# Optimization experiments

Measured on AMD Instinct MI355X. Metric: run time of the kernel, lower is better.

## Reference

```python
import jax, jax.numpy as jnp
import numpy as np

B, N, E = 2, 50000, 400000
FIN, HID, OUT = 128, 128, 128
EPS = 1e-5  # BatchNorm1d default eps


def setup_inputs() -> dict:
    key = jax.random.key(0)
    ks = jax.random.split(key, 12)
    x = jax.random.normal(ks[0], (B, N, FIN), dtype=jnp.float32)
    row = jax.random.randint(ks[1], (E,), 0, N, dtype=jnp.int32)          # scatter dst
    col = jnp.concatenate([jnp.arange(N, dtype=jnp.int32),                # ensure deg>=1
                           jax.random.randint(ks[2], (E - N,), 0, N, dtype=jnp.int32)])
    edge_index = jnp.stack([row, col])                                    # [2, E]
    deg = jnp.zeros((N,), jnp.float32).at[col].add(1.0)                   # degree(col, N)
    dis = deg ** -0.5
    norm = (dis[row] * dis[col])[None, :, None]                           # [1, E, 1]
    W1 = jax.random.normal(ks[3], (HID, FIN), jnp.float32) / np.sqrt(FIN)
    b1 = jax.random.normal(ks[4], (HID,), jnp.float32) * 0.01
    g1 = jnp.ones((N,), jnp.float32)
    be1 = jnp.zeros((N,), jnp.float32)
    W2 = jax.random.normal(ks[5], (OUT, HID), jnp.float32) / np.sqrt(HID)
    b2 = jax.random.normal(ks[6], (OUT,), jnp.float32) * 0.01
    g2 = jnp.ones((N,), jnp.float32)
    be2 = jnp.zeros((N,), jnp.float32)
    return {"x": x, "edge_index": edge_index, "norm": norm,
            "W1": W1, "b1": b1, "g1": g1, "be1": be1,
            "W2": W2, "b2": b2, "g2": g2, "be2": be2}


def _gcn_layer(x, edge_index, norm, W, b, g, be):
    # Linear (dropout p=0 -> identity)
    h = jnp.einsum('bnf,of->bno', x, W) + b                 # [B, N, C]
    # BatchNorm1d(num_features=N): per-node stats over (batch, channel)
    mu = jnp.mean(h, axis=(0, 2), keepdims=True)            # [1, N, 1]
    var = jnp.var(h, axis=(0, 2), keepdims=True)            # biased, as torch
    y = g[None, :, None] * (h - mu) * jax.lax.rsqrt(var + EPS) + be[None, :, None]
    a = jax.nn.gelu(y, approximate=False)                   # torch GELU = exact erf
    # message passing: gather src nodes, scale by norm, scatter-add to dst
    msgs = a[:, edge_index[1], :] * norm                    # [B, E, C]
    return jnp.zeros_like(a).at[:, edge_index[0], :].add(msgs)


def reference(x, edge_index, norm, W1, b1, g1, be1, W2, b2, g2, be2):
    x = _gcn_layer(x, edge_index, norm, W1, b1, g1, be1)
    x = _gcn_layer(x, edge_index, norm, W2, b2, g2, be2)
    return x
```

## Files before the change

kernel.cpp:

```cpp
#include <hip/hip_runtime.h>
#include <math.h>

#define CC 128

typedef unsigned short u16;
typedef short bf16x8 __attribute__((ext_vector_type(8)));
typedef float f32x4 __attribute__((ext_vector_type(4)));

typedef __attribute__((address_space(3))) void lds_t;
typedef const __attribute__((address_space(1))) void gbl_t;

__device__ __forceinline__ u16 f2bf(float f) {
    union { float f; unsigned u; } v; v.f = f;
    unsigned u = v.u;
    return (u16)((u + 0x7FFFu + ((u >> 16) & 1u)) >> 16);
}
__device__ __forceinline__ float bf2f(unsigned hi16) {
    union { unsigned u; float f; } v; v.u = hi16 << 16; return v.f;
}
__device__ __forceinline__ unsigned cvt_pk(float lo, float hi) {
    unsigned r;
    asm("v_cvt_pk_bf16_f32 %0, %1, %2" : "=v"(r) : "v"(lo), "v"(hi));
    return r;
}

__device__ __forceinline__ float gelu_f(float y) {
    float xa = fabsf(y) * 0.70710678118654752f;
    float t  = __builtin_amdgcn_rcpf(fmaf(0.3275911f, xa, 1.0f));
    float p  = fmaf(1.061405429f, t, -1.453152027f);
    p = fmaf(p, t, 1.421413741f);
    p = fmaf(p, t, -0.284496736f);
    p = fmaf(p, t, 0.254829592f);
    p *= t;
    float e  = __expf(-xa * xa);
    float er = fmaf(-p, e, 1.0f);
    float s  = copysignf(er, y);
    return 0.5f * y * (1.0f + s);
}


__global__ __launch_bounds__(256) void k_zero_i32(int* __restrict__ p, int n) {
    int i = blockIdx.x * 256 + threadIdx.x;
    if (i < n) p[i] = 0;
}

__global__ __launch_bounds__(256) void k_hist(const int* __restrict__ row, int* __restrict__ cnt, int E) {
    int e = blockIdx.x * 256 + threadIdx.x;
    if (e < E) atomicAdd(&cnt[row[e]], 1);
}

__device__ __forceinline__ int wave_incl_scan(int v) {
    #pragma unroll
    for (int d = 1; d < 64; d <<= 1) {
        int t = __shfl_up(v, d);
        if ((threadIdx.x & 63) >= d) v += t;
    }
    return v;
}

__global__ __launch_bounds__(256) void k_scan_a(const int* __restrict__ cnt, int* __restrict__ bsum, int N) {
    int base = blockIdx.x * 1024 + threadIdx.x * 4;
    int s = 0;
    #pragma unroll
    for (int u = 0; u < 4; ++u) { int i = base + u; if (i < N) s += cnt[i]; }
    #pragma unroll
    for (int d = 32; d > 0; d >>= 1) s += __shfl_down(s, d);
    __shared__ int wsum[4];
    if ((threadIdx.x & 63) == 0) wsum[threadIdx.x >> 6] = s;
    __syncthreads();
    if (threadIdx.x == 0) bsum[blockIdx.x] = wsum[0] + wsum[1] + wsum[2] + wsum[3];
}

__global__ __launch_bounds__(64) void k_scan_b(const int* __restrict__ bsum, int* __restrict__ boff,
                                               int* __restrict__ off, int N, int nb) {
    int carry = 0;
    for (int base = 0; base < nb; base += 64) {
        int t = base + (int)threadIdx.x;
        int v = (t < nb) ? bsum[t] : 0;
        int incl = wave_incl_scan(v);
        if (t < nb) boff[t] = carry + incl - v;
        carry += __shfl(incl, 63);
    }
    if (threadIdx.x == 0) off[N] = carry;
}

__global__ __launch_bounds__(256) void k_scan_c(int* __restrict__ cnt, const int* __restrict__ boff,
                                                int* __restrict__ off, int N) {
    int t = threadIdx.x;
    int base = blockIdx.x * 1024 + t * 4;
    int v[4]; int s = 0;
    #pragma unroll
    for (int u = 0; u < 4; ++u) { int i = base + u; v[u] = (i < N) ? cnt[i] : 0; s += v[u]; }
    int incl = wave_incl_scan(s);
    __shared__ int wsum[4];
    int w = t >> 6, lane = t & 63;
    if (lane == 63) wsum[w] = incl;
    __syncthreads();
    int run = incl - s + boff[blockIdx.x];
    for (int ww = 0; ww < w; ++ww) run += wsum[ww];
    #pragma unroll
    for (int u = 0; u < 4; ++u) {
        int i = base + u;
        if (i < N) { off[i] = run; cnt[i] = 0; }
        run += v[u];
    }
}

__global__ __launch_bounds__(256) void k_fill(const int* __restrict__ row, const int* __restrict__ col,
                                              const float* __restrict__ nrm, const int* __restrict__ off,
                                              int* __restrict__ cur, int2* __restrict__ eg, int E) {
    int e = blockIdx.x * 256 + threadIdx.x;
    if (e < E) {
        int r = row[e];
        int p = off[r] + atomicAdd(&cur[r], 1);
        eg[p] = make_int2(col[e], __float_as_int(nrm[e]));
    }
}

__global__ __launch_bounds__(256) void k_wrepack(const float* __restrict__ W1, u16* __restrict__ Wp1,
                                                 const float* __restrict__ W2, u16* __restrict__ Wp2) {
    int i = blockIdx.x * 256 + threadIdx.x;
    if (i < 2 * CC * CC) {
        int is2 = (i >= CC * CC);
        int ii = is2 ? i - CC * CC : i;
        int j = ii & 7, l = (ii >> 3) & 63, s = (ii >> 9) & 3, t = ii >> 11;
        int r = 16 * t + (l & 15);
        int p = s * 32 + ((l >> 4) & 3) * 8 + j;
        if (is2) {
            int k = (p & 7) * 16 + (p >> 3);
            Wp2[ii] = f2bf(W2[r * CC + k]);
        } else {
            Wp1[ii] = f2bf(W1[r * CC + p]);
        }
    }
}

__global__ __launch_bounds__(256) void k_fused_l1(
    const float* __restrict__ X, const u16* __restrict__ Wp1, const u16* __restrict__ Wp2,
    const float* __restrict__ bias, const float* __restrict__ gamma, const float* __restrict__ beta,
    u16* __restrict__ Z, int N)
{
    __shared__ __align__(16) u16 WS[CC * CC];
    __shared__ __align__(16) unsigned TT[4][16][68];

    const int tid = threadIdx.x;
    const int w = tid >> 6;
    const int l = tid & 63;
    const int g = l >> 4;
    const int c = l & 15;
    const int n8 = blockIdx.x * 32 + w * 8;
    const bool valid = n8 < N;
    const int nbase = valid ? n8 : 0;

    #pragma unroll
    for (int it = 0; it < 8; ++it) {
        const u16* gsrc = Wp1 + it * 2048 + w * 512 + l * 8;
        u16* ldst = &WS[it * 2048 + w * 512];
        __builtin_amdgcn_global_load_lds((gbl_t*)gsrc, (lds_t*)ldst, 16, 0, 0);
    }

    const int ab = c >> 3;
    const int an = nbase + (c & 7);
    const float* xbase = X + ((size_t)ab * N + an) * CC + g * 8;
    bf16x8 af[4];
    #pragma unroll
    for (int s = 0; s < 4; ++s) {
        float4 lo = *(const float4*)(xbase + s * 32);
        float4 hi = *(const float4*)(xbase + s * 32 + 4);
        unsigned aw[4];
        aw[0] = cvt_pk(lo.x, lo.y); aw[1] = cvt_pk(lo.z, lo.w);
        aw[2] = cvt_pk(hi.x, hi.y); aw[3] = cvt_pk(hi.z, hi.w);
        af[s] = *(bf16x8*)aw;
    }

    float bb[8];
    #pragma unroll
    for (int t = 0; t < 8; ++t) bb[t] = bias[t * 16 + c];
    float gam[4], bet[4];
    #pragma unroll
    for (int r = 0; r < 4; ++r) {
        int p = (4 * g + r) & 7;
        gam[r] = gamma[nbase + p];
        bet[r] = beta[nbase + p];
    }

    __syncthreads();

    f32x4 acc[8];
    #pragma unroll
    for (int t = 0; t < 8; ++t) acc[t] = (f32x4){0.f, 0.f, 0.f, 0.f};
    #pragma unroll
    for (int s = 0; s < 4; ++s) {
        bf16x8 bf[8];
        #pragma unroll
        for (int t = 0; t < 8; ++t)
            bf[t] = *(const bf16x8*)&WS[((t * 4 + s) * 64 + l) * 8];
        #pragma unroll
        for (int t = 0; t < 8; ++t)
            acc[t] = __builtin_amdgcn_mfma_f32_16x16x32_bf16(af[s], bf[t], acc[t], 0, 0, 0);
    }

    __syncthreads();

    #pragma unroll
    for (int it = 0; it < 8; ++it) {
        const u16* gsrc = Wp2 + it * 2048 + w * 512 + l * 8;
        u16* ldst = &WS[it * 2048 + w * 512];
        __builtin_amdgcn_global_load_lds((gbl_t*)gsrc, (lds_t*)ldst, 16, 0, 0);
    }

    float rs[4] = {0.f, 0.f, 0.f, 0.f}, rq[4] = {0.f, 0.f, 0.f, 0.f};
    #pragma unroll
    for (int t = 0; t < 8; ++t)
        #pragma unroll
        for (int r = 0; r < 4; ++r) {
            float h = acc[t][r] + bb[t];
            acc[t][r] = h;
            rs[r] += h;
            rq[r] += h * h;
        }
    #pragma unroll
    for (int d = 1; d < 16; d <<= 1) {
        #pragma unroll
        for (int r = 0; r < 4; ++r) {
            rs[r] += __shfl_xor(rs[r], d);
            rq[r] += __shfl_xor(rq[r], d);
        }
    }
    #pragma unroll
    for (int r = 0; r < 4; ++r) {
        rs[r] += __shfl_xor(rs[r], 32);
        rq[r] += __shfl_xor(rq[r], 32);
    }

    #pragma unroll
    for (int r = 0; r < 4; ++r) {
        float mean = rs[r] * (1.f / 256.f);
        float var  = rq[r] * (1.f / 256.f) - mean * mean;
        float sc = gam[r] * rsqrtf(fmaxf(var, 0.f) + 1e-5f);
        float sh = bet[r] - mean * sc;
        #pragma unroll
        for (int t = 0; t < 8; ++t)
            acc[t][r] = gelu_f(acc[t][r] * sc + sh);
    }

    #pragma unroll
    for (int r = 0; r < 4; ++r) {
        unsigned tw[4];
        #pragma unroll
        for (int tt = 0; tt < 4; ++tt)
            tw[tt] = cvt_pk(acc[2 * tt][r], acc[2 * tt + 1][r]);
        *(uint4*)&TT[w][4 * g + r][c * 4] = *(uint4*)tw;
    }
    bf16x8 af2[4];
    #pragma unroll
    for (int s = 0; s < 4; ++s)
        af2[s] = *(const bf16x8*)&TT[w][c][s * 16 + g * 4];

    __syncthreads();

    f32x4 acc2[8];
    #pragma unroll
    for (int t = 0; t < 8; ++t) acc2[t] = (f32x4){0.f, 0.f, 0.f, 0.f};
    #pragma unroll
    for (int s = 0; s < 4; ++s) {
        bf16x8 bf[8];
        #pragma unroll
        for (int t = 0; t < 8; ++t)
            bf[t] = *(const bf16x8*)&WS[((t * 4 + s) * 64 + l) * 8];
        #pragma unroll
        for (int t = 0; t < 8; ++t)
            acc2[t] = __builtin_amdgcn_mfma_f32_16x16x32_bf16(af2[s], bf[t], acc2[t], 0, 0, 0);
    }

    if (valid) {
        #pragma unroll
        for (int r = 0; r < 4; ++r) {
            int rr = 4 * g + r;
            int db = rr >> 3, dn = n8 + (rr & 7);
            unsigned zw[4];
            #pragma unroll
            for (int tt = 0; tt < 4; ++tt)
                zw[tt] = cvt_pk(acc2[2 * tt][r], acc2[2 * tt + 1][r]);
            *(uint4*)(Z + ((size_t)dn * 2 + db) * CC + c * 8) = *(uint4*)zw;
        }
    }
}

__global__ __launch_bounds__(256) void k_agg_bn(
    const u16* __restrict__ Zin, const int* __restrict__ off, const int2* __restrict__ eg,
    const float* __restrict__ b2, const float* __restrict__ g2, const float* __restrict__ be2,
    u16* __restrict__ A2, int N)
{
    __shared__ u16 TW[4][2][256];
    const int wv = threadIdx.x >> 6;
    const int l = threadIdx.x & 63;
    const int half = l >> 5;
    const int h = l & 31;
    const int b = h >> 4;
    const int c = h & 15;
    const int n = blockIdx.x * 8 + wv * 2 + half;
    const bool nv = n < N;
    const int nn = nv ? n : 0;
    const u16* Ab = Zin + b * CC + c * 8;

    float bb[8];
    #pragma unroll
    for (int t = 0; t < 8; ++t) bb[t] = b2[t * 16 + c];

    int s = off[nn];
    int e = nv ? off[nn + 1] : 0;
    float a[8] = {0.f, 0.f, 0.f, 0.f, 0.f, 0.f, 0.f, 0.f};
    for (int j = s; j < e; j += 4) {
        int2 e0 = eg[j], e1 = eg[j + 1], e2 = eg[j + 2], e3 = eg[j + 3];
        int s0 = e0.x;                  float w0 = __int_as_float(e0.y);
        int s1 = (j + 1 < e) ? e1.x : 0; float w1 = (j + 1 < e) ? __int_as_float(e1.y) : 0.f;
        int s2 = (j + 2 < e) ? e2.x : 0; float w2 = (j + 2 < e) ? __int_as_float(e2.y) : 0.f;
        int s3 = (j + 3 < e) ? e3.x : 0; float w3 = (j + 3 < e) ? __int_as_float(e3.y) : 0.f;
        bf16x8 v0 = *(const bf16x8*)(Ab + (size_t)s0 * 256);
        bf16x8 v1 = *(const bf16x8*)(Ab + (size_t)s1 * 256);
        bf16x8 v2 = *(const bf16x8*)(Ab + (size_t)s2 * 256);
        bf16x8 v3 = *(const bf16x8*)(Ab + (size_t)s3 * 256);
        #pragma unroll
        for (int q = 0; q < 8; ++q) {
            a[q] = fmaf(w0, bf2f((u16)v0[q]), a[q]);
            a[q] = fmaf(w1, bf2f((u16)v1[q]), a[q]);
            a[q] = fmaf(w2, bf2f((u16)v2[q]), a[q]);
            a[q] = fmaf(w3, bf2f((u16)v3[q]), a[q]);
        }
    }

    float ss = 0.f, qq = 0.f;
    #pragma unroll
    for (int t = 0; t < 8; ++t) {
        float hh = a[t] + bb[t];
        a[t] = hh;
        ss += hh;
        qq += hh * hh;
    }
    #pragma unroll
    for (int d = 1; d < 32; d <<= 1) {
        ss += __shfl_xor(ss, d);
        qq += __shfl_xor(qq, d);
    }
    float mean = ss * (1.f / 256.f);
    float var  = qq * (1.f / 256.f) - mean * mean;
    float sc = g2[nn] * rsqrtf(fmaxf(var, 0.f) + 1e-5f);
    float sh = be2[nn] - mean * sc;

    #pragma unroll
    for (int t = 0; t < 8; ++t)
        TW[wv][half][b * CC + t * 16 + c] = f2bf(gelu_f(a[t] * sc + sh));
    if (nv) {
        bf16x8 v = *(const bf16x8*)&TW[wv][half][h * 8];
        *(bf16x8*)(A2 + (size_t)nn * 256 + h * 8) = v;
    }
}

__global__ __launch_bounds__(256) void k_agg_out(
    const u16* __restrict__ A2, const int* __restrict__ off, const int2* __restrict__ eg,
    float* __restrict__ Out, int N)
{
    const int wv = threadIdx.x >> 6;
    const int l = threadIdx.x & 63;
    const int half = l >> 5;
    const int h = l & 31;
    const int b = h >> 4;
    const int c = h & 15;
    const int n = blockIdx.x * 8 + wv * 2 + half;
    const bool nv = n < N;
    const int nn = nv ? n : 0;
    const u16* Ab = A2 + h * 8;

    int s = off[nn];
    int e = nv ? off[nn + 1] : 0;
    float a[8] = {0.f, 0.f, 0.f, 0.f, 0.f, 0.f, 0.f, 0.f};
    for (int j = s; j < e; j += 4) {
        int2 e0 = eg[j], e1 = eg[j + 1], e2 = eg[j + 2], e3 = eg[j + 3];
        int s0 = e0.x;                  float w0 = __int_as_float(e0.y);
        int s1 = (j + 1 < e) ? e1.x : 0; float w1 = (j + 1 < e) ? __int_as_float(e1.y) : 0.f;
        int s2 = (j + 2 < e) ? e2.x : 0; float w2 = (j + 2 < e) ? __int_as_float(e2.y) : 0.f;
        int s3 = (j + 3 < e) ? e3.x : 0; float w3 = (j + 3 < e) ? __int_as_float(e3.y) : 0.f;
        bf16x8 v0 = *(const bf16x8*)(Ab + (size_t)s0 * 256);
        bf16x8 v1 = *(const bf16x8*)(Ab + (size_t)s1 * 256);
        bf16x8 v2 = *(const bf16x8*)(Ab + (size_t)s2 * 256);
        bf16x8 v3 = *(const bf16x8*)(Ab + (size_t)s3 * 256);
        #pragma unroll
        for (int q = 0; q < 8; ++q) {
            a[q] = fmaf(w0, bf2f((u16)v0[q]), a[q]);
            a[q] = fmaf(w1, bf2f((u16)v1[q]), a[q]);
            a[q] = fmaf(w2, bf2f((u16)v2[q]), a[q]);
            a[q] = fmaf(w3, bf2f((u16)v3[q]), a[q]);
        }
    }
    if (nv) {
        float* d = Out + ((size_t)b * N + nn) * CC + c * 8;
        *(float4*)&d[0] = make_float4(a[0], a[1], a[2], a[3]);
        *(float4*)&d[4] = make_float4(a[4], a[5], a[6], a[7]);
    }
}


extern "C" void kernel_launch(void* const* d_in, const int* in_sizes, int n_in,
                              void* d_out, int out_size, void* d_ws, size_t ws_size,
                              hipStream_t stream)
{
    const float* x   = (const float*)d_in[0];
    const int*   ei  = (const int*)d_in[1];
    const float* nrm = (const float*)d_in[2];
    const float* W1  = (const float*)d_in[3];
    const float* b1  = (const float*)d_in[4];
    const float* g1  = (const float*)d_in[5];
    const float* be1 = (const float*)d_in[6];
    const float* W2  = (const float*)d_in[7];
    const float* b2  = (const float*)d_in[8];
    const float* g2  = (const float*)d_in[9];
    const float* be2 = (const float*)d_in[10];

    const int N = in_sizes[5];
    const int E = in_sizes[2];
    const int* row = ei;
    const int* col = ei + E;
    const int nb = (N + 1023) / 1024;

    auto al = [](size_t v) { return (v + 255) & ~(size_t)255; };
    char* p = (char*)d_ws;
    int* off    = (int*)p;   p += al((size_t)(N + 1) * 4);
    int* cur    = (int*)p;   p += al((size_t)N * 4);
    int2* eg    = (int2*)p;  p += al((size_t)(E + 8) * 8);
    int* bsum   = (int*)p;   p += al((size_t)nb * 4);
    int* boff   = (int*)p;   p += al((size_t)nb * 4);
    u16* Wp1    = (u16*)p;   p += al((size_t)CC * CC * 2);
    u16* Wp2    = (u16*)p;   p += al((size_t)CC * CC * 2);
    u16* Zbuf   = (u16*)p;   p += al((size_t)2 * N * CC * 2);
    u16* A2buf  = (u16*)p;   p += al((size_t)2 * N * CC * 2);

    k_zero_i32<<<(N + 255) / 256, 256, 0, stream>>>(cur, N);
    k_hist<<<(E + 255) / 256, 256, 0, stream>>>(row, cur, E);
    k_scan_a<<<nb, 256, 0, stream>>>(cur, bsum, N);
    k_scan_b<<<1, 64, 0, stream>>>(bsum, boff, off, N, nb);
    k_scan_c<<<nb, 256, 0, stream>>>(cur, boff, off, N);
    k_fill<<<(E + 255) / 256, 256, 0, stream>>>(row, col, nrm, off, cur, eg, E);

    k_wrepack<<<(2 * CC * CC + 255) / 256, 256, 0, stream>>>(W1, Wp1, W2, Wp2);

    const int gb = (N + 31) / 32;
    const int ga = (N + 7) / 8;
    k_fused_l1<<<gb, 256, 0, stream>>>(x, Wp1, Wp2, b1, g1, be1, Zbuf, N);
    k_agg_bn<<<ga, 256, 0, stream>>>(Zbuf, off, eg, b2, g2, be2, A2buf, N);
    k_agg_out<<<ga, 256, 0, stream>>>(A2buf, off, eg, (float*)d_out, N);
}
```

Baseline: 153.2 us.

## Make fused layer-1 kernel persistent with resident weights and X prefetch

The fused linear/BN/GELU/linear kernel becomes persistent: 512 blocks loop over node tiles, keeping both repacked weight matrices in separate LDS buffers so they load once per block instead of once per tile. The next tile's X, gamma and beta are prefetched into registers while the current tile computes, and the transpose scratch uses an XOR swizzle instead of padding to avoid bank conflicts. The zeroing and weight-repack kernels are merged into one launch. The trade-offs are higher LDS and register use per block (launch_bounds 256,2) and a fixed grid size that may not match the CU count.

```diff
diff --git a/kernel.cpp b/kernel.cpp
--- a/kernel.cpp
+++ b/kernel.cpp
@@ -39,11 +39,6 @@
 }
 
 
-__global__ __launch_bounds__(256) void k_zero_i32(int* __restrict__ p, int n) {
-    int i = blockIdx.x * 256 + threadIdx.x;
-    if (i < n) p[i] = 0;
-}
-
 __global__ __launch_bounds__(256) void k_hist(const int* __restrict__ row, int* __restrict__ cnt, int E) {
     int e = blockIdx.x * 256 + threadIdx.x;
     if (e < E) atomicAdd(&cnt[row[e]], 1);
@@ -117,12 +112,15 @@
     }
 }
 
-__global__ __launch_bounds__(256) void k_wrepack(const float* __restrict__ W1, u16* __restrict__ Wp1,
-                                                 const float* __restrict__ W2, u16* __restrict__ Wp2) {
+__global__ __launch_bounds__(256) void k_prep(int* __restrict__ cur, int N,
+                                              const float* __restrict__ W1, u16* __restrict__ Wp1,
+                                              const float* __restrict__ W2, u16* __restrict__ Wp2) {
     int i = blockIdx.x * 256 + threadIdx.x;
-    if (i < 2 * CC * CC) {
-        int is2 = (i >= CC * CC);
-        int ii = is2 ? i - CC * CC : i;
+    if (i < N) { cur[i] = 0; return; }
+    int iw = i - N;
+    if (iw < 2 * CC * CC) {
+        int is2 = (iw >= CC * CC);
+        int ii = is2 ? iw - CC * CC : iw;
         int j = ii & 7, l = (ii >> 3) & 63, s = (ii >> 9) & 3, t = ii >> 11;
         int r = 16 * t + (l & 15);
         int p = s * 32 + ((l >> 4) & 3) * 8 + j;
@@ -135,154 +133,166 @@
     }
 }
 
-__global__ __launch_bounds__(256) void k_fused_l1(
+__global__ __launch_bounds__(256, 2) void k_fused_l1(
     const float* __restrict__ X, const u16* __restrict__ Wp1, const u16* __restrict__ Wp2,
     const float* __restrict__ bias, const float* __restrict__ gamma, const float* __restrict__ beta,
     u16* __restrict__ Z, int N)
 {
-    __shared__ __align__(16) u16 WS[CC * CC];
-    __shared__ __align__(16) unsigned TT[4][16][68];
+    __shared__ __align__(16) u16 WS1[CC * CC];
+    __shared__ __align__(16) u16 WS2[CC * CC];
+    __shared__ __align__(16) unsigned TT[4][16][64];
 
     const int tid = threadIdx.x;
     const int w = tid >> 6;
     const int l = tid & 63;
     const int g = l >> 4;
     const int c = l & 15;
-    const int n8 = blockIdx.x * 32 + w * 8;
-    const bool valid = n8 < N;
-    const int nbase = valid ? n8 : 0;
+    const int ntiles = (N + 31) / 32;
+    const int NB = gridDim.x;
 
     #pragma unroll
     for (int it = 0; it < 8; ++it) {
-        const u16* gsrc = Wp1 + it * 2048 + w * 512 + l * 8;
-        u16* ldst = &WS[it * 2048 + w * 512];
-        __builtin_amdgcn_global_load_lds((gbl_t*)gsrc, (lds_t*)ldst, 16, 0, 0);
-    }
-
-    const int ab = c >> 3;
-    const int an = nbase + (c & 7);
-    const float* xbase = X + ((size_t)ab * N + an) * CC + g * 8;
-    bf16x8 af[4];
-    #pragma unroll
-    for (int s = 0; s < 4; ++s) {
-        float4 lo = *(const float4*)(xbase + s * 32);
-        float4 hi = *(const float4*)(xbase + s * 32 + 4);
-        unsigned aw[4];
-        aw[0] = cvt_pk(lo.x, lo.y); aw[1] = cvt_pk(lo.z, lo.w);
-        aw[2] = cvt_pk(hi.x, hi.y); aw[3] = cvt_pk(hi.z, hi.w);
-        af[s] = *(bf16x8*)aw;
+        const u16* g1s = Wp1 + it * 2048 + w * 512 + l * 8;
+        const u16* g2s = Wp2 + it * 2048 + w * 512 + l * 8;
+        __builtin_amdgcn_global_load_lds((gbl_t*)g1s, (lds_t*)&WS1[it * 2048 + w * 512], 16, 0, 0);
+        __builtin_amdgcn_global_load_lds((gbl_t*)g2s, (lds_t*)&WS2[it * 2048 + w * 512], 16, 0, 0);
     }
 
     float bb[8];
     #pragma unroll
     for (int t = 0; t < 8; ++t) bb[t] = bias[t * 16 + c];
-    float gam[4], bet[4];
-    #pragma unroll
-    for (int r = 0; r < 4; ++r) {
-        int p = (4 * g + r) & 7;
-        gam[r] = gamma[nbase + p];
-        bet[r] = beta[nbase + p];
-    }
+
+    float4 xlo[4], xhi[4];
+    float gamv[4], betv[4];
+    auto prefetch = [&](int tt) {
+        int n8 = tt * 32 + w * 8;
+        int nb_ = (n8 < N) ? n8 : 0;
+        const float* xb = X + ((size_t)(c >> 3) * N + nb_ + (c & 7)) * CC + g * 8;
+        #pragma unroll
+        for (int s = 0; s < 4; ++s) {
+            xlo[s] = *(const float4*)(xb + s * 32);
+            xhi[s] = *(const float4*)(xb + s * 32 + 4);
+        }
+        #pragma unroll
+        for (int r = 0; r < 4; ++r) {
+            int p = (4 * g + r) & 7;
+            gamv[r] = gamma[nb_ + p];
+            betv[r] = beta[nb_ + p];
+        }
+    };
+    prefetch(blockIdx.x);
 
     __syncthreads();
 
-    f32x4 acc[8];
-    #pragma unroll
-    for (int t = 0; t < 8; ++t) acc[t] = (f32x4){0.f, 0.f, 0.f, 0.f};
-    #pragma unroll
-    for (int s = 0; s < 4; ++s) {
-        bf16x8 bf[8];
-        #pragma unroll
-        for (int t = 0; t < 8; ++t)
-            bf[t] = *(const bf16x8*)&WS[((t * 4 + s) * 64 + l) * 8];
-        #pragma unroll
-        for (int t = 0; t < 8; ++t)
-            acc[t] = __builtin_amdgcn_mfma_f32_16x16x32_bf16(af[s], bf[t], acc[t], 0, 0, 0);
-    }
-
-    __syncthreads();
-
-    #pragma unroll
-    for (int it = 0; it < 8; ++it) {
-        const u16* gsrc = Wp2 + it * 2048 + w * 512 + l * 8;
-        u16* ldst = &WS[it * 2048 + w * 512];
-        __builtin_amdgcn_global_load_lds((gbl_t*)gsrc, (lds_t*)ldst, 16, 0, 0);
-    }
-
-    float rs[4] = {0.f, 0.f, 0.f, 0.f}, rq[4] = {0.f, 0.f, 0.f, 0.f};
-    #pragma unroll
-    for (int t = 0; t < 8; ++t)
+    for (int t = blockIdx.x; t < ntiles; t += NB) {
+        const int n8 = t * 32 + w * 8;
+        const bool valid = n8 < N;
+
+        bf16x8 af[4];
+        #pragma unroll
+        for (int s = 0; s < 4; ++s) {
+            unsigned aw[4];
+            aw[0] = cvt_pk(xlo[s].x, xlo[s].y); aw[1] = cvt_pk(xlo[s].z, xlo[s].w);
+            aw[2] = cvt_pk(xhi[s].x, xhi[s].y); aw[3] = cvt_pk(xhi[s].z, xhi[s].w);
+            af[s] = *(bf16x8*)aw;
+        }
+        float gam[4], bet[4];
+        #pragma unroll
+        for (int r = 0; r < 4; ++r) { gam[r] = gamv[r]; bet[r] = betv[r]; }
+
+        if (t + NB < ntiles) prefetch(t + NB);
+
+        f32x4 acc[8];
+        #pragma unroll
+        for (int q = 0; q < 8; ++q) acc[q] = (f32x4){0.f, 0.f, 0.f, 0.f};
+        #pragma unroll
+        for (int s = 0; s < 4; ++s) {
+            bf16x8 bf[8];
+            #pragma unroll
+            for (int q = 0; q < 8; ++q)
+                bf[q] = *(const bf16x8*)&WS1[((q * 4 + s) * 64 + l) * 8];
+            #pragma unroll
+            for (int q = 0; q < 8; ++q)
+                acc[q] = __builtin_amdgcn_mfma_f32_16x16x32_bf16(af[s], bf[q], acc[q], 0, 0, 0);
+        }
+
+        float rs[4] = {0.f, 0.f, 0.f, 0.f}, rq[4] = {0.f, 0.f, 0.f, 0.f};
+        #pragma unroll
+        for (int q = 0; q < 8; ++q)
+            #pragma unroll
+            for (int r = 0; r < 4; ++r) {
+                float h = acc[q][r] + bb[q];
+                acc[q][r] = h;
+                rs[r] += h;
+                rq[r] += h * h;
+            }
+        #pragma unroll
+        for (int d = 1; d < 16; d <<= 1) {
+            #pragma unroll
+            for (int r = 0; r < 4; ++r) {
+                rs[r] += __shfl_xor(rs[r], d);
+                rq[r] += __shfl_xor(rq[r], d);
+            }
+        }
         #pragma unroll
         for (int r = 0; r < 4; ++r) {
-            float h = acc[t][r] + bb[t];
-            acc[t][r] = h;
-            rs[r] += h;
-            rq[r] += h * h;
-        }
-    #pragma unroll
-    for (int d = 1; d < 16; d <<= 1) {
+            rs[r] += __shfl_xor(rs[r], 32);
+            rq[r] += __shfl_xor(rq[r], 32);
+        }
+
         #pragma unroll
         for (int r = 0; r < 4; ++r) {
-            rs[r] += __shfl_xor(rs[r], d);
-            rq[r] += __shfl_xor(rq[r], d);
-        }
-    }
-    #pragma unroll
-    for (int r = 0; r < 4; ++r) {
-        rs[r] += __shfl_xor(rs[r], 32);
-        rq[r] += __shfl_xor(rq[r], 32);
-    }
-
-    #pragma unroll
-    for (int r = 0; r < 4; ++r) {
-        float mean = rs[r] * (1.f / 256.f);
-        float var  = rq[r] * (1.f / 256.f) - mean * mean;
-        float sc = gam[r] * rsqrtf(fmaxf(var, 0.f) + 1e-5f);
-        float sh = bet[r] - mean * sc;
-        #pragma unroll
-        for (int t = 0; t < 8; ++t)
-            acc[t][r] = gelu_f(acc[t][r] * sc + sh);
-    }
-
-    #pragma unroll
-    for (int r = 0; r < 4; ++r) {
-        unsigned tw[4];
-        #pragma unroll
-        for (int tt = 0; tt < 4; ++tt)
-            tw[tt] = cvt_pk(acc[2 * tt][r], acc[2 * tt + 1][r]);
-        *(uint4*)&TT[w][4 * g + r][c * 4] = *(uint4*)tw;
-    }
-    bf16x8 af2[4];
-    #pragma unroll
-    for (int s = 0; s < 4; ++s)
-        af2[s] = *(const bf16x8*)&TT[w][c][s * 16 + g * 4];
-
-    __syncthreads();
-
-    f32x4 acc2[8];
-    #pragma unroll
-    for (int t = 0; t < 8; ++t) acc2[t] = (f32x4){0.f, 0.f, 0.f, 0.f};
-    #pragma unroll
-    for (int s = 0; s < 4; ++s) {
-        bf16x8 bf[8];
-        #pragma unroll
-        for (int t = 0; t < 8; ++t)
-            bf[t] = *(const bf16x8*)&WS[((t * 4 + s) * 64 + l) * 8];
-        #pragma unroll
-        for (int t = 0; t < 8; ++t)
-            acc2[t] = __builtin_amdgcn_mfma_f32_16x16x32_bf16(af2[s], bf[t], acc2[t], 0, 0, 0);
-    }
-
-    if (valid) {
+            float mean = rs[r] * (1.f / 256.f);
+            float var  = rq[r] * (1.f / 256.f) - mean * mean;
+            float sc = gam[r] * rsqrtf(fmaxf(var, 0.f) + 1e-5f);
+            float sh = bet[r] - mean * sc;
+            #pragma unroll
+            for (int q = 0; q < 8; ++q)
+                acc[q][r] = gelu_f(acc[q][r] * sc + sh);
+        }
+
         #pragma unroll
         for (int r = 0; r < 4; ++r) {
-            int rr = 4 * g + r;
-            int db = rr >> 3, dn = n8 + (rr & 7);
-            unsigned zw[4];
+            int row = 4 * g + r;
+            unsigned tw[4];
             #pragma unroll
             for (int tt = 0; tt < 4; ++tt)
-                zw[tt] = cvt_pk(acc2[2 * tt][r], acc2[2 * tt + 1][r]);
-            *(uint4*)(Z + ((size_t)dn * 2 + db) * CC + c * 8) = *(uint4*)zw;
+                tw[tt] = cvt_pk(acc[2 * tt][r], acc[2 * tt + 1][r]);
+            int colw = (c * 4) ^ ((row & 7) << 2);
+            *(uint4*)&TT[w][row][colw] = *(uint4*)tw;
+        }
+        bf16x8 af2[4];
+        #pragma unroll
+        for (int s = 0; s < 4; ++s) {
+            int colr = (s * 16 + g * 4) ^ ((c & 7) << 2);
+            af2[s] = *(const bf16x8*)&TT[w][c][colr];
+        }
+
+        f32x4 acc2[8];
+        #pragma unroll
+        for (int q = 0; q < 8; ++q) acc2[q] = (f32x4){0.f, 0.f, 0.f, 0.f};
+        #pragma unroll
+        for (int s = 0; s < 4; ++s) {
+            bf16x8 bf[8];
+            #pragma unroll
+            for (int q = 0; q < 8; ++q)
+                bf[q] = *(const bf16x8*)&WS2[((q * 4 + s) * 64 + l) * 8];
+            #pragma unroll
+            for (int q = 0; q < 8; ++q)
+                acc2[q] = __builtin_amdgcn_mfma_f32_16x16x32_bf16(af2[s], bf[q], acc2[q], 0, 0, 0);
+        }
+
+        if (valid) {
+            #pragma unroll
+            for (int r = 0; r < 4; ++r) {
+                int rr = 4 * g + r;
+                int db = rr >> 3, dn = n8 + (rr & 7);
+                unsigned zw[4];
+                #pragma unroll
+                for (int tt = 0; tt < 4; ++tt)
+                    zw[tt] = cvt_pk(acc2[2 * tt][r], acc2[2 * tt + 1][r]);
+                *(uint4*)(Z + ((size_t)dn * 2 + db) * CC + c * 8) = *(uint4*)zw;
+            }
         }
     }
 }
@@ -435,18 +445,16 @@
     u16* Zbuf   = (u16*)p;   p += al((size_t)2 * N * CC * 2);
     u16* A2buf  = (u16*)p;   p += al((size_t)2 * N * CC * 2);
 
-    k_zero_i32<<<(N + 255) / 256, 256, 0, stream>>>(cur, N);
+    const int prep_n = N + 2 * CC * CC;
+    k_prep<<<(prep_n + 255) / 256, 256, 0, stream>>>(cur, N, W1, Wp1, W2, Wp2);
     k_hist<<<(E + 255) / 256, 256, 0, stream>>>(row, cur, E);
     k_scan_a<<<nb, 256, 0, stream>>>(cur, bsum, N);
     k_scan_b<<<1, 64, 0, stream>>>(bsum, boff, off, N, nb);
     k_scan_c<<<nb, 256, 0, stream>>>(cur, boff, off, N);
     k_fill<<<(E + 255) / 256, 256, 0, stream>>>(row, col, nrm, off, cur, eg, E);
 
-    k_wrepack<<<(2 * CC * CC + 255) / 256, 256, 0, stream>>>(W1, Wp1, W2, Wp2);
-
-    const int gb = (N + 31) / 32;
     const int ga = (N + 7) / 8;
-    k_fused_l1<<<gb, 256, 0, stream>>>(x, Wp1, Wp2, b1, g1, be1, Zbuf, N);
+    k_fused_l1<<<512, 256, 0, stream>>>(x, Wp1, Wp2, b1, g1, be1, Zbuf, N);
     k_agg_bn<<<ga, 256, 0, stream>>>(Zbuf, off, eg, b2, g2, be2, A2buf, N);
     k_agg_out<<<ga, 256, 0, stream>>>(A2buf, off, eg, (float*)d_out, N);
 }
```

New measurement: 150.2 us. 2.0% less time.
